# Performance work log

Measured on AMD Instinct MI355X. Metric: run time of the kernel, lower is better.

Reference implementation:

```python
import jax, jax.numpy as jnp
import numpy as np

L = 64          # lattice side
NSITES = L * L  # 4096
HALF = NSITES // 2
B = 16384
H = 128         # hidden width of s/t MLPs
SLOPE = 0.2     # tf.nn.leaky_relu default alpha

# checkerboard parity indices (static, evenodd = 0)
_coords = np.arange(NSITES)
_parity = (_coords // L + _coords % L) % 2
IDX_A = jnp.asarray(np.where(_parity == 0)[0], dtype=jnp.int32)  # [HALF]
IDX_B = jnp.asarray(np.where(_parity == 1)[0], dtype=jnp.int32)  # [HALF]


def setup_inputs() -> dict:
    key = jax.random.key(0)
    ks = jax.random.split(key, 8)
    scale = 0.05  # small init keeps exp(-s) well-behaved
    return {
        "z":    jax.random.normal(ks[0], (B, NSITES), dtype=jnp.float32),
        "s_W0": jax.random.normal(ks[1], (HALF, H), dtype=jnp.float32) * scale,
        "s_W1": jax.random.normal(ks[2], (H, H), dtype=jnp.float32) * scale,
        "s_W2": jax.random.normal(ks[3], (H, HALF), dtype=jnp.float32) * scale,
        "s_b2": jnp.zeros((HALF,), dtype=jnp.float32),
        "t_W0": jax.random.normal(ks[4], (HALF, H), dtype=jnp.float32) * scale,
        "t_W1": jax.random.normal(ks[5], (H, H), dtype=jnp.float32) * scale,
        "t_W2": jax.random.normal(ks[6], (H, HALF), dtype=jnp.float32) * scale,
        "t_b2": jnp.zeros((HALF,), dtype=jnp.float32),
    }


def _mlp(x, W0, W1, W2, b2):
    # Dense(no bias)+leaky_relu x2, then Dense(with bias), matching the keras stack
    h = jax.nn.leaky_relu(x @ W0, negative_slope=SLOPE)
    h = jax.nn.leaky_relu(h @ W1, negative_slope=SLOPE)
    return h @ W2 + b2


def reference(z, s_W0, s_W1, s_W2, s_b2, t_W0, t_W1, t_W2, t_b2):
    z_a = z[:, IDX_A]                       # [B, HALF] gather (even sites)
    z_b = z[:, IDX_B]                       # [B, HALF] gather (odd sites)
    s_out = _mlp(z_a, s_W0, s_W1, s_W2, s_b2)   # [B, HALF]
    t_a = _mlp(z_a, t_W0, t_W1, t_W2, t_b2)     # [B, HALF]
    s_a = jnp.exp(-s_out)
    f_b = (z_b - t_a) * s_a                 # affine coupling
    # scatter back (disjoint indices -> set is equivalent to scatter_nd add)
    f = jnp.zeros_like(z).at[:, IDX_A].set(z_a).at[:, IDX_B].set(f_b)
    d = jnp.sum(s_out, axis=1)              # logdetjacfwd: sum of s(z_a)
    return (f, d)
```

## Files before the change

kernel.cpp:

```cpp
#include <hip/hip_runtime.h>
#include <hip/hip_bf16.h>

#define BATCH  16384
#define SLOPE  0.2f
#define BM     32

typedef __attribute__((ext_vector_type(8))) short bf16x8;
typedef __attribute__((ext_vector_type(4))) float f32x4;
typedef __attribute__((ext_vector_type(4))) float fx4;
typedef __attribute__((ext_vector_type(2))) float fx2;

#define OFF_SW0T 0
#define OFF_TW0T 262144
#define OFF_SW1T 524288
#define OFF_TW1T 540672
#define OFF_SW2T 557056
#define OFF_TW2T 819200

__device__ __forceinline__ unsigned short f2bf(float f) {
    unsigned int u = __float_as_uint(f);
    u += 0x7FFFu + ((u >> 16) & 1u);
    return (unsigned short)(u >> 16);
}

__global__ void conv_w(const float* __restrict__ sW0, const float* __restrict__ sW1,
                       const float* __restrict__ sW2, const float* __restrict__ tW0,
                       const float* __restrict__ tW1, const float* __restrict__ tW2,
                       unsigned short* __restrict__ ws) {
    const int total = 262144 + 16384 + 262144;
    for (int i = blockIdx.x * blockDim.x + threadIdx.x; i < total;
         i += gridDim.x * blockDim.x) {
        if (i < 262144) {
            int k = i >> 7, n = i & 127;
            int ks = (k & ~63) | ((((k >> 3) & 7) ^ (n & 7)) << 3) | (k & 7);
            ws[OFF_SW0T + n * 2048 + ks] = f2bf(sW0[i]);
            ws[OFF_TW0T + n * 2048 + ks] = f2bf(tW0[i]);
        } else if (i < 262144 + 16384) {
            int j = i - 262144;
            int k = j >> 7, n = j & 127;
            ws[OFF_SW1T + n * 128 + k] = f2bf(sW1[j]);
            ws[OFF_TW1T + n * 128 + k] = f2bf(tW1[j]);
        } else {
            int j = i - (262144 + 16384);
            int k = j >> 11, n = j & 2047;
            int ks = ((((k >> 3) & 15) ^ (n & 7)) << 3) | (k & 7);
            ws[OFF_SW2T + n * 128 + ks] = f2bf(sW2[j]);
            ws[OFF_TW2T + n * 128 + ks] = f2bf(tW2[j]);
        }
    }
}

__global__ __launch_bounds__(256, 2) void coupling_main(
    const float* __restrict__ z,
    const float* __restrict__ s_b2,
    const float* __restrict__ t_b2,
    const unsigned short* __restrict__ ws,
    float* __restrict__ f_out,
    float* __restrict__ d_vec) {

    __shared__ __align__(16) unsigned char LDSbuf[73728];
    unsigned short* HA = (unsigned short*)(LDSbuf + 8192);
    unsigned short* HB = (unsigned short*)(LDSbuf + 24576);
    float* Dred = (float*)(LDSbuf + 65536);

    const int tid  = threadIdx.x;
    const int wave = tid >> 6;
    const int lane = tid & 63;
    const int l15  = lane & 15;
    const int l4   = lane >> 4;
    const int brow = blockIdx.x * BM;

    const char* wsb = (const char*)ws;
    const fx4* __restrict__ zf4 = (const fx4*)z;
    const fx2* __restrict__ zf2 = (const fx2*)z;
    fx2* __restrict__ ff2 = (fx2*)f_out;

    auto ldzTo = [&](fx4 (&zr)[4], int c) {
        #pragma unroll
        for (int q = 0; q < 4; ++q) {
            const int f = tid + 256 * q;
            const int row = f >> 5, col16 = f & 31;
            zr[q] = __builtin_nontemporal_load(
                zf4 + (size_t)(brow + row) * 1024 + c * 32 + col16);
        }
    };
    auto wrzFrom = [&](fx4 (&zr)[4], int b) {
        #pragma unroll
        for (int q = 0; q < 4; ++q) {
            const int f = tid + 256 * q;
            const int row = f >> 5, col16 = f & 31;
            const int par = (col16 >> 4) & 1;
            const float a0 = par ? zr[q].y : zr[q].x;
            const float a1 = par ? zr[q].w : zr[q].z;
            const unsigned int pk = (unsigned int)f2bf(a0) | ((unsigned int)f2bf(a1) << 16);
            *(unsigned int*)(LDSbuf + b * 4096 + row * 128 +
                             (((col16 >> 2) ^ (row & 7)) << 4) + (col16 & 3) * 4) = pk;
        }
    };
    auto stageW0 = [&](int b, int c) {
        #pragma unroll
        for (int jj = 0; jj < 8; ++jj) {
            const char* g = wsb + (size_t)(wave * 64 + jj * 8 + (lane >> 3)) * 4096
                            + c * 128 + (lane & 7) * 16;
            void* l = LDSbuf + 8192 + b * 32768 + (wave * 64 + jj * 8) * 128;
            __builtin_amdgcn_global_load_lds(
                (const __attribute__((address_space(1))) unsigned int*)g,
                (__attribute__((address_space(3))) unsigned int*)l, 16, 0, 0);
        }
    };

    f32x4 acc0[2][4] = {};
    auto cmp0 = [&](int cb) {
        const char* Az = (const char*)(LDSbuf + cb * 4096);
        const char* Wt = (const char*)(LDSbuf + 8192 + cb * 32768);
        bf16x8 af[2][2], wf[4][2];
        #pragma unroll
        for (int m = 0; m < 2; ++m)
            #pragma unroll
            for (int k2 = 0; k2 < 2; ++k2) {
                const int row = m * 16 + l15;
                af[m][k2] = *(const bf16x8*)(Az + row * 128 +
                              ((k2 * 64 + l4 * 16) ^ ((row & 7) << 4)));
            }
        #pragma unroll
        for (int n2 = 0; n2 < 4; ++n2)
            #pragma unroll
            for (int k2 = 0; k2 < 2; ++k2) {
                const int g = wave * 64 + n2 * 16 + l15;
                wf[n2][k2] = *(const bf16x8*)(Wt + g * 128 +
                               ((k2 * 64 + l4 * 16) ^ ((g & 7) << 4)));
            }
        #pragma unroll
        for (int n2 = 0; n2 < 4; ++n2)
            #pragma unroll
            for (int k2 = 0; k2 < 2; ++k2)
                #pragma unroll
                for (int m = 0; m < 2; ++m)
                    acc0[m][n2] = __builtin_amdgcn_mfma_f32_16x16x32_bf16(
                        af[m][k2], wf[n2][k2], acc0[m][n2], 0, 0, 0);
    };

    fx4 zA[4], zB[4];
    auto phase = [&](int p, int cb, fx4 (&zLd)[4], fx4 (&zWr)[4]) {
        if (p + 1 < 32) stageW0(cb ^ 1, p + 1);
        if (p + 2 < 32) ldzTo(zLd, p + 2);
        if (p <= 29)
            asm volatile("s_waitcnt vmcnt(16)" ::: "memory");
        else if (p == 30)
            asm volatile("s_waitcnt vmcnt(12)" ::: "memory");
        else
            asm volatile("s_waitcnt vmcnt(0)" ::: "memory");
        cmp0(cb);
        if (p + 1 < 32) wrzFrom(zWr, cb ^ 1);
        asm volatile("s_waitcnt lgkmcnt(0)" ::: "memory");
        __builtin_amdgcn_s_barrier();
        __builtin_amdgcn_sched_barrier(0);
    };

    ldzTo(zB, 0);
    stageW0(0, 0);
    wrzFrom(zB, 0);
    ldzTo(zB, 1);
    asm volatile("s_waitcnt lgkmcnt(0)" ::: "memory");
    __builtin_amdgcn_s_barrier();
    __builtin_amdgcn_sched_barrier(0);

    #pragma unroll 1
    for (int gIt = 0; gIt < 16; ++gIt) {
        phase(2 * gIt,     0, zA, zB);
        phase(2 * gIt + 1, 1, zB, zA);
    }

    #pragma unroll
    for (int m = 0; m < 2; ++m)
        #pragma unroll
        for (int n2 = 0; n2 < 4; ++n2)
            #pragma unroll
            for (int r = 0; r < 4; ++r) {
                float v = acc0[m][n2][r];
                v = v > 0.0f ? v : SLOPE * v;
                const int row = m * 16 + l4 * 4 + r;
                const int col = wave * 64 + n2 * 16 + l15;
                HA[row * 256 + (col ^ ((row & 7) << 3))] = f2bf(v);
            }
    __syncthreads();

    f32x4 acc1[2][4] = {};
    const int net1 = wave >> 1;
    #pragma unroll
    for (int k4 = 0; k4 < 4; ++k4) {
        bf16x8 ahv[2];
        #pragma unroll
        for (int m = 0; m < 2; ++m) {
            const int row = m * 16 + l15;
            ahv[m] = *(const bf16x8*)&HA[row * 256 +
                       ((net1 * 128 + k4 * 32 + l4 * 8) ^ ((row & 7) << 3))];
        }
        #pragma unroll
        for (int n2 = 0; n2 < 4; ++n2) {
            const bf16x8 w = *(const bf16x8*)&ws[OFF_SW1T +
                (size_t)(wave * 64 + n2 * 16 + l15) * 128 + k4 * 32 + l4 * 8];
            #pragma unroll
            for (int m = 0; m < 2; ++m)
                acc1[m][n2] = __builtin_amdgcn_mfma_f32_16x16x32_bf16(
                    ahv[m], w, acc1[m][n2], 0, 0, 0);
        }
    }
    __syncthreads();
    #pragma unroll
    for (int m = 0; m < 2; ++m)
        #pragma unroll
        for (int n2 = 0; n2 < 4; ++n2)
            #pragma unroll
            for (int r = 0; r < 4; ++r) {
                float v = acc1[m][n2][r];
                v = v > 0.0f ? v : SLOPE * v;
                const int row = m * 16 + l4 * 4 + r;
                const int col = wave * 64 + n2 * 16 + l15;
                HB[row * 256 + (col ^ ((row & 7) << 3))] = f2bf(v);
            }
    __syncthreads();

    const int par = wave >> 1;

    bf16x8 ahs[2][4], aht[2][4];
    #pragma unroll
    for (int m = 0; m < 2; ++m)
        #pragma unroll
        for (int k4 = 0; k4 < 4; ++k4) {
            const int row = m * 16 + l15;
            const int kc = k4 * 32 + l4 * 8;
            ahs[m][k4] = *(const bf16x8*)&HB[row * 256 + (kc ^ ((row & 7) << 3))];
            aht[m][k4] = *(const bf16x8*)&HB[row * 256 + ((128 + kc) ^ ((row & 7) << 3))];
        }
    __syncthreads();

    auto stageW2 = [&](int b, int c2) {
        #pragma unroll
        for (int jj = 0; jj < 8; ++jj) {
            const int net  = jj >> 2;
            const int rloc = wave * 16 + (jj & 3) * 4 + (lane >> 4);
            const int pr   = c2 * 64 + rloc;
            const char* g = wsb + (size_t)(net ? OFF_TW2T : OFF_SW2T) * 2
                            + (size_t)pr * 256 + (lane & 15) * 16;
            void* l = LDSbuf + b * 32768 + (net * 64 + wave * 16 + (jj & 3) * 4) * 256;
            __builtin_amdgcn_global_load_lds(
                (const __attribute__((address_space(1))) unsigned int*)g,
                (__attribute__((address_space(3))) unsigned int*)l, 16, 0, 0);
        }
    };

    float dsum[2][4] = {};

    fx2 zvA[2][4], zvB[2][4];
    float sbA, tbA, sbB, tbB;
    auto ldzEp = [&](fx2 (&zv)[2][4], float& sb, float& tb, int c2) {
        const int j = c2 * 64 + wave * 16 + l15;
        sb = s_b2[j];
        tb = t_b2[j];
        #pragma unroll
        for (int m = 0; m < 2; ++m)
            #pragma unroll
            for (int r = 0; r < 4; ++r)
                zv[m][r] = __builtin_nontemporal_load(
                    &zf2[(size_t)(brow + m * 16 + l4 * 4 + r) * 2048 + j]);
    };

    auto l2body = [&](fx2 (&zv)[2][4], float sb, float tb, int c2, int cb) {
        bf16x8 wfs[4], wft[4];
        #pragma unroll
        for (int k4 = 0; k4 < 4; ++k4) {
            const int rs = wave * 16 + l15;
            const int rt = 64 + wave * 16 + l15;
            const int kc = k4 * 64 + l4 * 16;
            wfs[k4] = *(const bf16x8*)(LDSbuf + cb * 32768 + rs * 256 + (kc ^ ((rs & 7) << 4)));
            wft[k4] = *(const bf16x8*)(LDSbuf + cb * 32768 + rt * 256 + (kc ^ ((rt & 7) << 4)));
        }
        f32x4 acc2[2][2] = {};
        #pragma unroll
        for (int k4 = 0; k4 < 4; ++k4)
            #pragma unroll
            for (int m = 0; m < 2; ++m) {
                acc2[0][m] = __builtin_amdgcn_mfma_f32_16x16x32_bf16(
                    ahs[m][k4], wfs[k4], acc2[0][m], 0, 0, 0);
                acc2[1][m] = __builtin_amdgcn_mfma_f32_16x16x32_bf16(
                    aht[m][k4], wft[k4], acc2[1][m], 0, 0, 0);
            }
        const int j = c2 * 64 + wave * 16 + l15;
        #pragma unroll
        for (int m = 0; m < 2; ++m)
            #pragma unroll
            for (int r = 0; r < 4; ++r) {
                const float sv = acc2[0][m][r] + sb;
                const float tv = acc2[1][m][r] + tb;
                const fx2 zp = zv[m][r];
                const float za = par ? zp.y : zp.x;
                const float zb = par ? zp.x : zp.y;
                const float fb = (zb - tv) * __expf(-sv);
                fx2 fv;
                if (par) { fv.x = fb; fv.y = za; }
                else     { fv.x = za; fv.y = fb; }
                __builtin_nontemporal_store(fv,
                    &ff2[(size_t)(brow + m * 16 + l4 * 4 + r) * 2048 + j]);
                dsum[m][r] += sv;
            }
    };

    stageW2(0, 0);
    ldzEp(zvA, sbA, tbA, 0);

    #pragma unroll 1
    for (int it = 0; it < 16; ++it) {
        {
            const int c2 = 2 * it;
            stageW2(1, c2 + 1);
            ldzEp(zvB, sbB, tbB, c2 + 1);
            if (c2 == 0)
                asm volatile("s_waitcnt vmcnt(28)" ::: "memory");
            else
                asm volatile("s_waitcnt vmcnt(36)" ::: "memory");
            l2body(zvA, sbA, tbA, c2, 0);
        }
        {
            const int c2 = 2 * it + 1;
            if (c2 < 31) {
                stageW2(0, c2 + 1);
                ldzEp(zvA, sbA, tbA, c2 + 1);
                asm volatile("s_waitcnt vmcnt(36)" ::: "memory");
            } else {
                asm volatile("s_waitcnt vmcnt(18)" ::: "memory");
            }
            l2body(zvB, sbB, tbB, c2, 1);
        }
    }

    #pragma unroll
    for (int m = 0; m < 2; ++m)
        #pragma unroll
        for (int r = 0; r < 4; ++r) {
            float v = dsum[m][r];
            v += __shfl_xor(v, 1);
            v += __shfl_xor(v, 2);
            v += __shfl_xor(v, 4);
            v += __shfl_xor(v, 8);
            if (l15 == 0) Dred[wave * 32 + m * 16 + l4 * 4 + r] = v;
        }
    __syncthreads();
    if (tid < BM)
        d_vec[brow + tid] = Dred[tid] + Dred[32 + tid] + Dred[64 + tid] + Dred[96 + tid];
}

extern "C" void kernel_launch(void* const* d_in, const int* in_sizes, int n_in,
                              void* d_out, int out_size, void* d_ws, size_t ws_size,
                              hipStream_t stream) {
    const float* z   = (const float*)d_in[0];
    const float* sW0 = (const float*)d_in[1];
    const float* sW1 = (const float*)d_in[2];
    const float* sW2 = (const float*)d_in[3];
    const float* sb2 = (const float*)d_in[4];
    const float* tW0 = (const float*)d_in[5];
    const float* tW1 = (const float*)d_in[6];
    const float* tW2 = (const float*)d_in[7];
    const float* tb2 = (const float*)d_in[8];

    float* fout = (float*)d_out;
    float* dvec = fout + (size_t)BATCH * 4096;
    unsigned short* ws = (unsigned short*)d_ws;

    hipLaunchKernelGGL(conv_w, dim3(512), dim3(256), 0, stream,
                       sW0, sW1, sW2, tW0, tW1, tW2, ws);
    hipLaunchKernelGGL(coupling_main, dim3(BATCH / BM), dim3(256), 0, stream,
                       z, sb2, tb2, ws, fout, dvec);
}
```

Measured before the change: 207.9 us.

## Single-buffer weight tiles in LDS to allow four blocks per CU

Weight staging for layers 0 and 2 moves from double-buffered LDS to a single buffer. Each wave now reads its fragments into registers, waits for LDS, and only then issues the next global-to-LDS copy. This cuts LDS from 72KB to 40KB, and launch bounds rise to 4 blocks per CU so more waves can hide memory latency. The trade-off is less prefetch distance per block and a tighter VGPR budget, which may cause spills. Waitcnt thresholds are retuned to match.

```diff
diff --git a/kernel.cpp b/kernel.cpp
--- a/kernel.cpp
+++ b/kernel.cpp
@@ -50,7 +50,7 @@
     }
 }
 
-__global__ __launch_bounds__(256, 2) void coupling_main(
+__global__ __launch_bounds__(256, 4) void coupling_main(
     const float* __restrict__ z,
     const float* __restrict__ s_b2,
     const float* __restrict__ t_b2,
@@ -58,10 +58,10 @@
     float* __restrict__ f_out,
     float* __restrict__ d_vec) {
 
-    __shared__ __align__(16) unsigned char LDSbuf[73728];
-    unsigned short* HA = (unsigned short*)(LDSbuf + 8192);
-    unsigned short* HB = (unsigned short*)(LDSbuf + 24576);
-    float* Dred = (float*)(LDSbuf + 65536);
+    __shared__ __align__(16) unsigned char LDSbuf[40960];
+    unsigned short* HA = (unsigned short*)(LDSbuf);
+    unsigned short* HB = (unsigned short*)(LDSbuf + 16384);
+    float* Dred = (float*)(LDSbuf + 32768);
 
     const int tid  = threadIdx.x;
     const int wave = tid >> 6;
@@ -97,12 +97,12 @@
                              (((col16 >> 2) ^ (row & 7)) << 4) + (col16 & 3) * 4) = pk;
         }
     };
-    auto stageW0 = [&](int b, int c) {
+    auto stageW0 = [&](int c) {
         #pragma unroll
         for (int jj = 0; jj < 8; ++jj) {
             const char* g = wsb + (size_t)(wave * 64 + jj * 8 + (lane >> 3)) * 4096
                             + c * 128 + (lane & 7) * 16;
-            void* l = LDSbuf + 8192 + b * 32768 + (wave * 64 + jj * 8) * 128;
+            void* l = LDSbuf + 8192 + (wave * 64 + jj * 8) * 128;
             __builtin_amdgcn_global_load_lds(
                 (const __attribute__((address_space(1))) unsigned int*)g,
                 (__attribute__((address_space(3))) unsigned int*)l, 16, 0, 0);
@@ -110,9 +110,11 @@
     };
 
     f32x4 acc0[2][4] = {};
-    auto cmp0 = [&](int cb) {
+
+    fx4 zA[4], zB[4];
+    auto phase = [&](int p, int cb, fx4 (&zLd)[4], fx4 (&zWr)[4]) {
         const char* Az = (const char*)(LDSbuf + cb * 4096);
-        const char* Wt = (const char*)(LDSbuf + 8192 + cb * 32768);
+        const char* Wt = (const char*)(LDSbuf + 8192);
         bf16x8 af[2][2], wf[4][2];
         #pragma unroll
         for (int m = 0; m < 2; ++m)
@@ -130,6 +132,9 @@
                 wf[n2][k2] = *(const bf16x8*)(Wt + g * 128 +
                                ((k2 * 64 + l4 * 16) ^ ((g & 7) << 4)));
             }
+        asm volatile("s_waitcnt lgkmcnt(0)" ::: "memory");
+        if (p + 1 < 32) stageW0(p + 1);
+        if (p + 2 < 32) ldzTo(zLd, p + 2);
         #pragma unroll
         for (int n2 = 0; n2 < 4; ++n2)
             #pragma unroll
@@ -138,30 +143,20 @@
                 for (int m = 0; m < 2; ++m)
                     acc0[m][n2] = __builtin_amdgcn_mfma_f32_16x16x32_bf16(
                         af[m][k2], wf[n2][k2], acc0[m][n2], 0, 0, 0);
-    };
-
-    fx4 zA[4], zB[4];
-    auto phase = [&](int p, int cb, fx4 (&zLd)[4], fx4 (&zWr)[4]) {
-        if (p + 1 < 32) stageW0(cb ^ 1, p + 1);
-        if (p + 2 < 32) ldzTo(zLd, p + 2);
-        if (p <= 29)
-            asm volatile("s_waitcnt vmcnt(16)" ::: "memory");
-        else if (p == 30)
-            asm volatile("s_waitcnt vmcnt(12)" ::: "memory");
+        if (p + 1 < 32) wrzFrom(zWr, cb ^ 1);
+        if (p + 2 < 32)
+            asm volatile("s_waitcnt lgkmcnt(0) vmcnt(4)" ::: "memory");
         else
-            asm volatile("s_waitcnt vmcnt(0)" ::: "memory");
-        cmp0(cb);
-        if (p + 1 < 32) wrzFrom(zWr, cb ^ 1);
-        asm volatile("s_waitcnt lgkmcnt(0)" ::: "memory");
+            asm volatile("s_waitcnt lgkmcnt(0) vmcnt(0)" ::: "memory");
         __builtin_amdgcn_s_barrier();
         __builtin_amdgcn_sched_barrier(0);
     };
 
     ldzTo(zB, 0);
-    stageW0(0, 0);
+    stageW0(0);
     wrzFrom(zB, 0);
     ldzTo(zB, 1);
-    asm volatile("s_waitcnt lgkmcnt(0)" ::: "memory");
+    asm volatile("s_waitcnt lgkmcnt(0) vmcnt(4)" ::: "memory");
     __builtin_amdgcn_s_barrier();
     __builtin_amdgcn_sched_barrier(0);
 
@@ -235,7 +230,7 @@
         }
     __syncthreads();
 
-    auto stageW2 = [&](int b, int c2) {
+    auto stageW2 = [&](int c2) {
         #pragma unroll
         for (int jj = 0; jj < 8; ++jj) {
             const int net  = jj >> 2;
@@ -243,7 +238,7 @@
             const int pr   = c2 * 64 + rloc;
             const char* g = wsb + (size_t)(net ? OFF_TW2T : OFF_SW2T) * 2
                             + (size_t)pr * 256 + (lane & 15) * 16;
-            void* l = LDSbuf + b * 32768 + (net * 64 + wave * 16 + (jj & 3) * 4) * 256;
+            void* l = LDSbuf + (net * 64 + wave * 16 + (jj & 3) * 4) * 256;
             __builtin_amdgcn_global_load_lds(
                 (const __attribute__((address_space(1))) unsigned int*)g,
                 (__attribute__((address_space(3))) unsigned int*)l, 16, 0, 0);
@@ -251,7 +246,6 @@
     };
 
     float dsum[2][4] = {};
-
     fx2 zvA[2][4], zvB[2][4];
     float sbA, tbA, sbB, tbB;
     auto ldzEp = [&](fx2 (&zv)[2][4], float& sb, float& tb, int c2) {
@@ -266,15 +260,25 @@
                     &zf2[(size_t)(brow + m * 16 + l4 * 4 + r) * 2048 + j]);
     };
 
-    auto l2body = [&](fx2 (&zv)[2][4], float sb, float tb, int c2, int cb) {
+    auto l2iter = [&](fx2 (&zvCur)[2][4], float sbC, float tbC,
+                      fx2 (&zvNxt)[2][4], float& sbN, float& tbN, int c2) {
+        if (c2 == 0)
+            asm volatile("s_waitcnt vmcnt(10)" ::: "memory");
+        else
+            asm volatile("s_waitcnt vmcnt(18)" ::: "memory");
         bf16x8 wfs[4], wft[4];
         #pragma unroll
         for (int k4 = 0; k4 < 4; ++k4) {
             const int rs = wave * 16 + l15;
             const int rt = 64 + wave * 16 + l15;
             const int kc = k4 * 64 + l4 * 16;
-            wfs[k4] = *(const bf16x8*)(LDSbuf + cb * 32768 + rs * 256 + (kc ^ ((rs & 7) << 4)));
-            wft[k4] = *(const bf16x8*)(LDSbuf + cb * 32768 + rt * 256 + (kc ^ ((rt & 7) << 4)));
+            wfs[k4] = *(const bf16x8*)(LDSbuf + rs * 256 + (kc ^ ((rs & 7) << 4)));
+            wft[k4] = *(const bf16x8*)(LDSbuf + rt * 256 + (kc ^ ((rt & 7) << 4)));
+        }
+        asm volatile("s_waitcnt lgkmcnt(0)" ::: "memory");
+        if (c2 + 1 < 32) {
+            stageW2(c2 + 1);
+            ldzEp(zvNxt, sbN, tbN, c2 + 1);
         }
         f32x4 acc2[2][2] = {};
         #pragma unroll
@@ -291,9 +295,9 @@
         for (int m = 0; m < 2; ++m)
             #pragma unroll
             for (int r = 0; r < 4; ++r) {
-                const float sv = acc2[0][m][r] + sb;
-                const float tv = acc2[1][m][r] + tb;
-                const fx2 zp = zv[m][r];
+                const float sv = acc2[0][m][r] + sbC;
+                const float tv = acc2[1][m][r] + tbC;
+                const fx2 zp = zvCur[m][r];
                 const float za = par ? zp.y : zp.x;
                 const float zb = par ? zp.x : zp.y;
                 const float fb = (zb - tv) * __expf(-sv);
@@ -306,34 +310,16 @@
             }
     };
 
-    stageW2(0, 0);
+    stageW2(0);
     ldzEp(zvA, sbA, tbA, 0);
 
     #pragma unroll 1
     for (int it = 0; it < 16; ++it) {
-        {
-            const int c2 = 2 * it;
-            stageW2(1, c2 + 1);
-            ldzEp(zvB, sbB, tbB, c2 + 1);
-            if (c2 == 0)
-                asm volatile("s_waitcnt vmcnt(28)" ::: "memory");
-            else
-                asm volatile("s_waitcnt vmcnt(36)" ::: "memory");
-            l2body(zvA, sbA, tbA, c2, 0);
-        }
-        {
-            const int c2 = 2 * it + 1;
-            if (c2 < 31) {
-                stageW2(0, c2 + 1);
-                ldzEp(zvA, sbA, tbA, c2 + 1);
-                asm volatile("s_waitcnt vmcnt(36)" ::: "memory");
-            } else {
-                asm volatile("s_waitcnt vmcnt(18)" ::: "memory");
-            }
-            l2body(zvB, sbB, tbB, c2, 1);
-        }
+        l2iter(zvA, sbA, tbA, zvB, sbB, tbB, 2 * it);
+        l2iter(zvB, sbB, tbB, zvA, sbA, tbA, 2 * it + 1);
     }
 
+    __syncthreads();
     #pragma unroll
     for (int m = 0; m < 2; ++m)
         #pragma unroll
```

Measured after the change: 628.4 us. 202% more time.
